# Kernel optimization log

Measured on AMD Instinct MI355X. Metric: run time of the kernel, lower is better.

The kernel has to match this reference:

```python
import jax, jax.numpy as jnp
import numpy as np

B, H, W, C_IN, C_QK = 8, 64, 64, 256, 32


def setup_inputs() -> dict:
    key = jax.random.key(0)
    ks = jax.random.split(key, 5)
    x = jax.random.normal(ks[0], (B, H, W, C_IN), dtype=jnp.float32)
    Wq = jax.random.normal(ks[1], (C_IN, C_QK), dtype=jnp.float32) * 0.05
    bq = jnp.zeros((C_QK,), dtype=jnp.float32)
    Wk = jax.random.normal(ks[2], (C_IN, C_QK), dtype=jnp.float32) * 0.05
    bk = jnp.zeros((C_QK,), dtype=jnp.float32)
    Wv = jax.random.normal(ks[3], (C_IN, C_IN), dtype=jnp.float32) * 0.05
    bv = jnp.zeros((C_IN,), dtype=jnp.float32)
    gamma = jax.random.normal(ks[4], (1,), dtype=jnp.float32)
    return {"x": x, "Wq": Wq, "bq": bq, "Wk": Wk, "bk": bk, "Wv": Wv, "bv": bv, "gamma": gamma}


def reference(x, Wq, bq, Wk, bk, Wv, bv, gamma):
    b, h, w, c_in = x.shape
    n = h * w
    xt = x.reshape(b, n, c_in)                      # tokens: (B, N, C_in)
    # 1x1 convs == per-token channel matmuls
    q = xt @ Wq + bq                                # (B, N, Cqk)
    k = xt @ Wk + bk                                # (B, N, Cqk)
    v = xt @ Wv + bv                                # (B, N, C_in)
    energy = jnp.einsum('bnc,bmc->bnm', q, k)       # (B, N, N)
    attn = jax.nn.softmax(energy, axis=-1)
    # original: out = (V^T @ A^T)^T == A @ V
    out = jnp.einsum('bnm,bmc->bnc', attn, v)       # (B, N, C_in)
    out = out.reshape(b, h, w, c_in)
    out = gamma * out + x                           # residual with learned scale
    return jnp.mean(out, axis=-1)                   # channel-mean pool -> (B, H, W)
```

## Files before the change

### kernel.cpp

```cpp
#include <hip/hip_runtime.h>
#include <hip/hip_bf16.h>


typedef _Float16 half8  __attribute__((ext_vector_type(8)));
typedef _Float16 half4v __attribute__((ext_vector_type(4)));
typedef float    f32x4  __attribute__((ext_vector_type(4)));

#define LOG2E 1.4426950408889634f

#if __has_builtin(__builtin_amdgcn_exp2f)
#define EXP2(x) __builtin_amdgcn_exp2f(x)
#else
#define EXP2(x) exp2f(x)
#endif

__global__ __launch_bounds__(256) void prep_kernel(
    const float* __restrict__ Wq, const float* __restrict__ Wk,
    const float* __restrict__ Wv, const float* __restrict__ bv,
    _Float16* __restrict__ Wfr, float* __restrict__ wvbar, float* __restrict__ bvbar)
{
  int bid = blockIdx.x, tid = threadIdx.x;
  if (bid < 64) {
    int col = bid, c = tid;
    float v = (col < 32) ? Wq[c * 32 + col] : Wk[c * 32 + (col - 32)];
    int ch = c >> 5, quad = (c >> 3) & 3, j = c & 7;
    Wfr[(size_t)((ch * 4 + quad) * 64 + col) * 8 + j] = (_Float16)v;
  } else if (bid < 128) {
    int row = (bid - 64) * 4 + (tid >> 6);
    int lane = tid & 63;
    const float* p = Wv + (size_t)row * 256 + lane * 4;
    float s = p[0] + p[1] + p[2] + p[3];
    #pragma unroll
    for (int off = 32; off >= 1; off >>= 1) s += __shfl_xor(s, off);
    if (lane == 0) wvbar[row] = s * (1.0f / 256.0f);
  } else {
    if (tid < 64) {
      const float* p = bv + tid * 4;
      float s = p[0] + p[1] + p[2] + p[3];
      #pragma unroll
      for (int off = 32; off >= 1; off >>= 1) s += __shfl_xor(s, off);
      if (tid == 0) bvbar[0] = s * (1.0f / 256.0f);
    }
  }
}

__global__ __launch_bounds__(256) void proj_kernel(
    const float* __restrict__ x, const _Float16* __restrict__ Wfr,
    const float* __restrict__ bq, const float* __restrict__ bk,
    const float* __restrict__ wvbar, const float* __restrict__ bvbar,
    _Float16* __restrict__ Qh, _Float16* __restrict__ Kh,
    float* __restrict__ vbarO, float* __restrict__ xbarO)
{
  __shared__ _Float16 XT[64 * 264];
  int tid = threadIdx.x, blk = blockIdx.x;
  size_t tok0 = (size_t)blk * 64;

  const float4* xg4 = (const float4*)x;
  #pragma unroll
  for (int i = 0; i < 16; ++i) {
    int f = i * 256 + tid;
    int tok = f >> 6, c4 = f & 63;
    float4 v = xg4[(size_t)blk * 4096 + f];
    half4v h;
    h.x = (_Float16)v.x; h.y = (_Float16)v.y; h.z = (_Float16)v.z; h.w = (_Float16)v.w;
    *(half4v*)&XT[tok * 264 + c4 * 4] = h;
  }
  __syncthreads();

  if (tid < 64) {
    float vs = 0.f, xs = 0.f;
    #pragma unroll 4
    for (int g = 0; g < 32; ++g) {
      half8 h = *(const half8*)&XT[tid * 264 + g * 8];
      #pragma unroll
      for (int j = 0; j < 8; ++j) {
        float xv = (float)h[j];
        vs += xv * wvbar[g * 8 + j];
        xs += xv;
      }
    }
    vbarO[tok0 + tid] = vs + bvbar[0];
    xbarO[tok0 + tid] = xs * (1.0f / 256.0f);
  }

  int lane = tid & 63, w = tid >> 6;
  int l15 = lane & 15, quad = lane >> 4;
  f32x4 acc[4] = {(f32x4){0,0,0,0},(f32x4){0,0,0,0},(f32x4){0,0,0,0},(f32x4){0,0,0,0}};
  #pragma unroll
  for (int ch = 0; ch < 8; ++ch) {
    half8 a = *(const half8*)&XT[(w * 16 + l15) * 264 + ch * 32 + quad * 8];
    #pragma unroll
    for (int ct = 0; ct < 4; ++ct) {
      half8 bf = *(const half8*)(Wfr + (size_t)((ch * 4 + quad) * 64 + ct * 16 + l15) * 8);
      acc[ct] = __builtin_amdgcn_mfma_f32_16x16x32_f16(a, bf, acc[ct], 0, 0, 0);
    }
  }
  #pragma unroll
  for (int ct = 0; ct < 4; ++ct) {
    int col = ct * 16 + l15;
    #pragma unroll
    for (int r = 0; r < 4; ++r) {
      int token = w * 16 + quad * 4 + r;
      if (ct < 2) {
        float val = (acc[ct][r] + bq[col]) * LOG2E;
        Qh[(tok0 + token) * 32 + col] = (_Float16)val;
      } else {
        float val = acc[ct][r] + bk[col - 32];
        Kh[(tok0 + token) * 32 + (col - 32)] = (_Float16)val;
      }
    }
  }
}

__global__ __launch_bounds__(256) void flash_kernel(
    const _Float16* __restrict__ Qh, const _Float16* __restrict__ Kh,
    const float* __restrict__ vbar, const float* __restrict__ xbar,
    const float* __restrict__ gamma, float* __restrict__ out)
{
  int tid = threadIdx.x, blk = blockIdx.x;
  int b = blk >> 6, qt = blk & 63;
  int lane = tid & 63, w = tid >> 6;
  int l15 = lane & 15, quad = lane >> 4;

  const _Float16* Qb = Qh + (size_t)b * 4096 * 32;
  const _Float16* Kb = Kh + (size_t)b * 4096 * 32;
  const float* vb = vbar + (size_t)b * 4096;

  int qrow = qt * 64 + w * 16 + l15;
  half8 aq = *(const half8*)(Qb + (size_t)qrow * 32 + quad * 8);

  float lacc[4] = {0, 0, 0, 0}, oacc[4] = {0, 0, 0, 0};
  const f32x4 cinit = {-88.f, -88.f, -88.f, -88.f};

  const _Float16* kfrag = Kb + (size_t)l15 * 32 + quad * 8;
  const float* vfrag = vb + l15;

  #pragma unroll 2
  for (int kt = 0; kt < 64; ++kt) {
    half8 bk8[4];
    float vbl[4];
    #pragma unroll
    for (int ct = 0; ct < 4; ++ct) {
      bk8[ct] = *(const half8*)(kfrag + (size_t)(kt * 64 + ct * 16) * 32);
      vbl[ct] = vfrag[kt * 64 + ct * 16];
    }
    f32x4 sc[4];
    #pragma unroll
    for (int ct = 0; ct < 4; ++ct)
      sc[ct] = __builtin_amdgcn_mfma_f32_16x16x32_f16(aq, bk8[ct], cinit, 0, 0, 0);
    #pragma unroll
    for (int r = 0; r < 4; ++r) {
      float p0 = EXP2(sc[0][r]), p1 = EXP2(sc[1][r]);
      float p2 = EXP2(sc[2][r]), p3 = EXP2(sc[3][r]);
      lacc[r] += (p0 + p1) + (p2 + p3);
      oacc[r] += ((p0 * vbl[0] + p1 * vbl[1]) + (p2 * vbl[2] + p3 * vbl[3]));
    }
  }

  #pragma unroll
  for (int r = 0; r < 4; ++r) {
    #pragma unroll
    for (int off = 1; off < 16; off <<= 1) {
      lacc[r] += __shfl_xor(lacc[r], off);
      oacc[r] += __shfl_xor(oacc[r], off);
    }
  }
  if (l15 == 0) {
    float g = gamma[0];
    #pragma unroll
    for (int r = 0; r < 4; ++r) {
      int row = qt * 64 + w * 16 + quad * 4 + r;
      out[(size_t)b * 4096 + row] = g * (oacc[r] / lacc[r]) + xbar[(size_t)b * 4096 + row];
    }
  }
}

extern "C" void kernel_launch(void* const* d_in, const int* in_sizes, int n_in,
                              void* d_out, int out_size, void* d_ws, size_t ws_size,
                              hipStream_t stream)
{
  const float* x     = (const float*)d_in[0];
  const float* Wq    = (const float*)d_in[1];
  const float* bq    = (const float*)d_in[2];
  const float* Wk    = (const float*)d_in[3];
  const float* bk    = (const float*)d_in[4];
  const float* Wv    = (const float*)d_in[5];
  const float* bv    = (const float*)d_in[6];
  const float* gamma = (const float*)d_in[7];
  float* out = (float*)d_out;

  char* ws = (char*)d_ws;
  _Float16* Wfr  = (_Float16*)(ws);
  float* wvbar   = (float*)(ws + 32768);
  float* bvbar   = (float*)(ws + 33792);
  _Float16* Qh   = (_Float16*)(ws + 65536);
  _Float16* Kh   = (_Float16*)(ws + 65536 + 2097152);
  float* vbarA   = (float*)(ws + 65536 + 4194304);
  float* xbarA   = (float*)(ws + 65536 + 4194304 + 131072);

  prep_kernel<<<129, 256, 0, stream>>>(Wq, Wk, Wv, bv, Wfr, wvbar, bvbar);
  proj_kernel<<<512, 256, 0, stream>>>(x, Wfr, bq, bk, wvbar, bvbar, Qh, Kh, vbarA, xbarA);
  flash_kernel<<<512, 256, 0, stream>>>(Qh, Kh, vbarA, xbarA, gamma, out);
}
```

Baseline: 125.6 us.

## Split attention key range across two blocks with combine kernel and prefetch

The flash kernel now splits each query tile's key range in half across two blocks, doubling the grid to 1024 blocks, and writes partial softmax sums and weighted sums to workspace. A new combine kernel adds the two halves and applies gamma and the residual mean. The inner loop also software-prefetches the next K/vbar fragments and uses packed float2 accumulation, with a launch-bounds occupancy hint added. This is meant to fill more CUs and hide load latency, at the cost of one extra kernel launch and a small partial-result round trip through memory.

After: 128.6 us. 2.4% more time.

```diff
diff --git a/kernel.cpp b/kernel.cpp
--- a/kernel.cpp
+++ b/kernel.cpp
@@ -5,6 +5,7 @@
 typedef _Float16 half8  __attribute__((ext_vector_type(8)));
 typedef _Float16 half4v __attribute__((ext_vector_type(4)));
 typedef float    f32x4  __attribute__((ext_vector_type(4)));
+typedef float    f32x2  __attribute__((ext_vector_type(2)));
 
 #define LOG2E 1.4426950408889634f
 
@@ -112,67 +113,94 @@
   }
 }
 
-__global__ __launch_bounds__(256) void flash_kernel(
+__global__ __launch_bounds__(256, 4) void flash_kernel(
     const _Float16* __restrict__ Qh, const _Float16* __restrict__ Kh,
-    const float* __restrict__ vbar, const float* __restrict__ xbar,
-    const float* __restrict__ gamma, float* __restrict__ out)
+    const float* __restrict__ vbar,
+    float* __restrict__ lpart, float* __restrict__ opart)
 {
   int tid = threadIdx.x, blk = blockIdx.x;
-  int b = blk >> 6, qt = blk & 63;
+  int ks = blk & 1, qt = (blk >> 1) & 63, b = blk >> 7;
   int lane = tid & 63, w = tid >> 6;
   int l15 = lane & 15, quad = lane >> 4;
 
   const _Float16* Qb = Qh + (size_t)b * 4096 * 32;
-  const _Float16* Kb = Kh + (size_t)b * 4096 * 32;
-  const float* vb = vbar + (size_t)b * 4096;
+  const _Float16* Kb = Kh + (size_t)b * 4096 * 32 + (size_t)ks * 2048 * 32;
+  const float* vb = vbar + (size_t)b * 4096 + ks * 2048;
 
   int qrow = qt * 64 + w * 16 + l15;
   half8 aq = *(const half8*)(Qb + (size_t)qrow * 32 + quad * 8);
 
-  float lacc[4] = {0, 0, 0, 0}, oacc[4] = {0, 0, 0, 0};
   const f32x4 cinit = {-88.f, -88.f, -88.f, -88.f};
-
   const _Float16* kfrag = Kb + (size_t)l15 * 32 + quad * 8;
   const float* vfrag = vb + l15;
 
-  #pragma unroll 2
-  for (int kt = 0; kt < 64; ++kt) {
-    half8 bk8[4];
-    float vbl[4];
-    #pragma unroll
-    for (int ct = 0; ct < 4; ++ct) {
-      bk8[ct] = *(const half8*)(kfrag + (size_t)(kt * 64 + ct * 16) * 32);
-      vbl[ct] = vfrag[kt * 64 + ct * 16];
-    }
-    f32x4 sc[4];
-    #pragma unroll
-    for (int ct = 0; ct < 4; ++ct)
-      sc[ct] = __builtin_amdgcn_mfma_f32_16x16x32_f16(aq, bk8[ct], cinit, 0, 0, 0);
+  f32x2 lacc[4] = {(f32x2){0,0},(f32x2){0,0},(f32x2){0,0},(f32x2){0,0}};
+  f32x2 oacc[4] = {(f32x2){0,0},(f32x2){0,0},(f32x2){0,0},(f32x2){0,0}};
+
+  half8 kc0, kc1, kc2, kc3;
+  float vc0, vc1, vc2, vc3;
+  kc0 = *(const half8*)(kfrag + 0 * 512);
+  kc1 = *(const half8*)(kfrag + 1 * 512);
+  kc2 = *(const half8*)(kfrag + 2 * 512);
+  kc3 = *(const half8*)(kfrag + 3 * 512);
+  vc0 = vfrag[0]; vc1 = vfrag[16]; vc2 = vfrag[32]; vc3 = vfrag[48];
+
+  for (int kt = 0; kt < 32; ++kt) {
+    half8 kn0, kn1, kn2, kn3;
+    float vn0, vn1, vn2, vn3;
+    if (kt < 31) {
+      const _Float16* kf = kfrag + (size_t)(kt + 1) * 2048;
+      const float* vf = vfrag + (kt + 1) * 64;
+      kn0 = *(const half8*)(kf + 0 * 512);
+      kn1 = *(const half8*)(kf + 1 * 512);
+      kn2 = *(const half8*)(kf + 2 * 512);
+      kn3 = *(const half8*)(kf + 3 * 512);
+      vn0 = vf[0]; vn1 = vf[16]; vn2 = vf[32]; vn3 = vf[48];
+    }
+    f32x4 s0 = __builtin_amdgcn_mfma_f32_16x16x32_f16(aq, kc0, cinit, 0, 0, 0);
+    f32x4 s1 = __builtin_amdgcn_mfma_f32_16x16x32_f16(aq, kc1, cinit, 0, 0, 0);
+    f32x4 s2 = __builtin_amdgcn_mfma_f32_16x16x32_f16(aq, kc2, cinit, 0, 0, 0);
+    f32x4 s3 = __builtin_amdgcn_mfma_f32_16x16x32_f16(aq, kc3, cinit, 0, 0, 0);
+    f32x2 va = {vc0, vc1}, vbp = {vc2, vc3};
     #pragma unroll
     for (int r = 0; r < 4; ++r) {
-      float p0 = EXP2(sc[0][r]), p1 = EXP2(sc[1][r]);
-      float p2 = EXP2(sc[2][r]), p3 = EXP2(sc[3][r]);
-      lacc[r] += (p0 + p1) + (p2 + p3);
-      oacc[r] += ((p0 * vbl[0] + p1 * vbl[1]) + (p2 * vbl[2] + p3 * vbl[3]));
-    }
+      f32x2 pa = {EXP2(s0[r]), EXP2(s1[r])};
+      f32x2 pb = {EXP2(s2[r]), EXP2(s3[r])};
+      lacc[r] += pa + pb;
+      oacc[r] += pa * va;
+      oacc[r] += pb * vbp;
+    }
+    kc0 = kn0; kc1 = kn1; kc2 = kn2; kc3 = kn3;
+    vc0 = vn0; vc1 = vn1; vc2 = vn2; vc3 = vn3;
   }
 
   #pragma unroll
   for (int r = 0; r < 4; ++r) {
+    float ls = lacc[r].x + lacc[r].y;
+    float os = oacc[r].x + oacc[r].y;
     #pragma unroll
     for (int off = 1; off < 16; off <<= 1) {
-      lacc[r] += __shfl_xor(lacc[r], off);
-      oacc[r] += __shfl_xor(oacc[r], off);
-    }
-  }
-  if (l15 == 0) {
-    float g = gamma[0];
-    #pragma unroll
-    for (int r = 0; r < 4; ++r) {
+      ls += __shfl_xor(ls, off);
+      os += __shfl_xor(os, off);
+    }
+    if (l15 == 0) {
       int row = qt * 64 + w * 16 + quad * 4 + r;
-      out[(size_t)b * 4096 + row] = g * (oacc[r] / lacc[r]) + xbar[(size_t)b * 4096 + row];
-    }
-  }
+      size_t idx = (size_t)ks * 32768 + (size_t)b * 4096 + row;
+      lpart[idx] = ls;
+      opart[idx] = os;
+    }
+  }
+}
+
+__global__ __launch_bounds__(256) void combine_kernel(
+    const float* __restrict__ lpart, const float* __restrict__ opart,
+    const float* __restrict__ xbar, const float* __restrict__ gamma,
+    float* __restrict__ out)
+{
+  int i = blockIdx.x * 256 + threadIdx.x;
+  float l = lpart[i] + lpart[32768 + i];
+  float o = opart[i] + opart[32768 + i];
+  out[i] = gamma[0] * (o / l) + xbar[i];
 }
 
 extern "C" void kernel_launch(void* const* d_in, const int* in_sizes, int n_in,
@@ -197,8 +225,11 @@
   _Float16* Kh   = (_Float16*)(ws + 65536 + 2097152);
   float* vbarA   = (float*)(ws + 65536 + 4194304);
   float* xbarA   = (float*)(ws + 65536 + 4194304 + 131072);
+  float* lpart   = (float*)(ws + 65536 + 4194304 + 262144);
+  float* opart   = (float*)(ws + 65536 + 4194304 + 524288);
 
   prep_kernel<<<129, 256, 0, stream>>>(Wq, Wk, Wv, bv, Wfr, wvbar, bvbar);
   proj_kernel<<<512, 256, 0, stream>>>(x, Wfr, bq, bk, wvbar, bvbar, Qh, Kh, vbarA, xbarA);
-  flash_kernel<<<512, 256, 0, stream>>>(Qh, Kh, vbarA, xbarA, gamma, out);
-}
+  flash_kernel<<<1024, 256, 0, stream>>>(Qh, Kh, vbarA, lpart, opart);
+  combine_kernel<<<128, 256, 0, stream>>>(lpart, opart, xbarA, gamma, out);
+}
```
